# Performance work log

Hardware: AMD Instinct MI355X
Metric: run time of the kernel (lower is better)

The kernel has to match this reference:

```python
import jax, jax.numpy as jnp
import numpy as np

BATCH, DIN, HID = 32768, 64, 1024


def setup_inputs() -> dict:
    key = jax.random.key(0)
    ks = jax.random.split(key, 8)
    s_in = 1.0 / np.sqrt(DIN)
    s_h = 1.0 / np.sqrt(HID)
    return {
        "z": jax.random.normal(ks[0], (BATCH, DIN), dtype=jnp.float32),
        # Hamiltonian net: DIN -> HID -> HID -> 1
        "W1": jax.random.normal(ks[1], (DIN, HID), dtype=jnp.float32) * s_in,
        "b1": jnp.zeros((HID,), jnp.float32),
        "W2": jax.random.normal(ks[2], (HID, HID), dtype=jnp.float32) * s_h,
        "b2": jnp.zeros((HID,), jnp.float32),
        "W3": jax.random.normal(ks[3], (HID, 1), dtype=jnp.float32) * s_h,
        "b3": jnp.zeros((1,), jnp.float32),
        # Forcing net: DIN -> HID -> DIN
        "Wf1": jax.random.normal(ks[4], (DIN, HID), dtype=jnp.float32) * s_in,
        "bf1": jnp.zeros((HID,), jnp.float32),
        "Wf2": jax.random.normal(ks[5], (HID, DIN), dtype=jnp.float32) * s_h,
        "bf2": jnp.zeros((DIN,), jnp.float32),
    }


def reference(z, W1, b1, W2, b2, W3, b3, Wf1, bf1, Wf2, bf2):
    def H_sum(zz):
        h1 = jnp.tanh(zz @ W1 + b1)          # [B, HID]
        h2 = jnp.tanh(h1 @ W2 + b2)          # [B, HID]
        return jnp.sum(h2 @ W3 + b3)         # scalar (sum of H over batch)

    gradH = jax.grad(H_sum)(z)               # [B, DIN]
    dim = z.shape[1] // 2
    # symplectic combine: dq/dt = dH/dp, dp/dt = -dH/dq
    hnn_term = jnp.concatenate([gradH[:, dim:], -gradH[:, :dim]], axis=-1)
    forcing_term = jnp.tanh(z @ Wf1 + bf1) @ Wf2 + bf2  # [B, DIN]
    return hnn_term + forcing_term
```

## Files before the change

### kernel.cpp

```cpp
#include <hip/hip_runtime.h>


typedef __attribute__((ext_vector_type(8))) short s16x8;
typedef __attribute__((ext_vector_type(4))) float f32x4;
typedef unsigned short u16;

#define DEVFN static __device__ __forceinline__

constexpr int DIN = 64;
constexpr int HID = 1024;

DEVFN u16 f2bf(float f) {
  unsigned u = __builtin_bit_cast(unsigned, f);
  u += 0x7fffu + ((u >> 16) & 1u);
  return (u16)(u >> 16);
}
DEVFN float bf2f(u16 h) {
  unsigned u = ((unsigned)h) << 16;
  return __builtin_bit_cast(float, u);
}
DEVFN float fast_tanh(float x) {
  float e = __builtin_amdgcn_exp2f(x * 2.8853900817779268f);
  return 1.0f - 2.0f * __builtin_amdgcn_rcpf(e + 1.0f);
}
DEVFN f32x4 mfma16(s16x8 a, s16x8 b, f32x4 c) {
  return __builtin_amdgcn_mfma_f32_16x16x32_bf16(a, b, c, 0, 0, 0);
}

#define GLOAD16(g, l) __builtin_amdgcn_global_load_lds( \
    (const __attribute__((address_space(1))) unsigned int*)(const void*)(g), \
    (__attribute__((address_space(3))) unsigned int*)(void*)(l), 16, 0, 0)

__global__ __launch_bounds__(256) void k0_w2(const float* __restrict__ W2,
                                             u16* __restrict__ W2tp, u16* __restrict__ W2c) {
  __shared__ u16 tl[64 * 65];
  const int bi = blockIdx.x >> 4, bj = blockIdx.x & 15;
  const int tid = threadIdx.x;
#pragma unroll
  for (int i = 0; i < 16; ++i) {
    int idx = i * 256 + tid;
    int r = idx >> 6, c = idx & 63;
    float v = W2[(size_t)(bi * 64 + r) * 1024 + bj * 64 + c];
    u16 b = f2bf(v);
    W2c[(size_t)(bi * 64 + r) * 1024 + bj * 64 + c] = b;
    tl[r * 65 + c] = b;
  }
  __syncthreads();
#pragma unroll
  for (int i = 0; i < 16; ++i) {
    int idx = i * 256 + tid;
    int r = idx >> 6, c = idx & 63;
    W2tp[(size_t)(bj * 64 + r) * 1024 + bi * 64 + c] = tl[c * 65 + r];
  }
}

__global__ __launch_bounds__(256) void k0_small(
    const float* W1, const float* Wf1, const float* Wf2,
    u16* W1p, u16* Wf1p, u16* W1s, u16* Wf2p) {
  int id = blockIdx.x * 256 + threadIdx.x;
  int n = id >> 6, k = id & 63;
  W1p[id]  = f2bf(W1[k * HID + n]);
  Wf1p[id] = f2bf(Wf1[k * HID + n]);
  int nn = id >> 10, kk2 = id & 1023;
  float s = (nn < 32) ? 1.f : -1.f;
  W1s[id]  = f2bf(s * W1[((nn + 32) & 63) * HID + kk2]);
  Wf2p[id] = f2bf(Wf2[kk2 * DIN + nn]);
}

__global__ __launch_bounds__(256) void k1_h1(const float* z, const u16* Wp,
                                             const float* b, u16* o) {
  __shared__ __align__(16) u16 zl[64 * 72];
  const int tid = threadIdx.x;
  const int lane = tid & 63, w = tid >> 6;
  const int nb = blockIdx.x & 7, mb = blockIdx.x >> 3;
  const size_t m0 = (size_t)mb * 64;
  const int n0 = nb * 128;
#pragma unroll
  for (int c = 0; c < 4; ++c) {
    int i4 = c * 256 + tid;
    int row = i4 >> 4, col4 = (i4 & 15) * 4;
    f32x4 v = *reinterpret_cast<const f32x4*>(z + (m0 + row) * DIN + col4);
    u16* d = zl + row * 72 + col4;
    d[0] = f2bf(v[0]); d[1] = f2bf(v[1]); d[2] = f2bf(v[2]); d[3] = f2bf(v[3]);
  }
  __syncthreads();
  f32x4 acc[8] = {};
#pragma unroll
  for (int kk = 0; kk < 2; ++kk) {
    const int karr = kk * 32 + ((lane >> 4) << 3);
    s16x8 a = *reinterpret_cast<const s16x8*>(zl + (16 * w + (lane & 15)) * 72 + karr);
#pragma unroll
    for (int fn = 0; fn < 8; ++fn) {
      int n = n0 + fn * 16 + (lane & 15);
      s16x8 bb = *reinterpret_cast<const s16x8*>(Wp + (size_t)n * 64 + karr);
      acc[fn] = mfma16(a, bb, acc[fn]);
    }
  }
#pragma unroll
  for (int fn = 0; fn < 8; ++fn) {
    int n = n0 + fn * 16 + (lane & 15);
    float bias = b[n];
#pragma unroll
    for (int j = 0; j < 4; ++j) {
      size_t m = m0 + 16 * w + ((lane >> 4) << 2) + j;
      o[m * HID + n] = f2bf(fast_tanh(acc[fn][j] + bias));
    }
  }
}

template <int MODE>
__global__ __launch_bounds__(512, 2) void k23_gemm(
    const u16* __restrict__ A, const u16* __restrict__ Bp,
    const float* __restrict__ b2, const float* __restrict__ W3,
    const u16* __restrict__ h1in, u16* __restrict__ outb) {
  extern __shared__ u16 lds[];
  const int tid = threadIdx.x;
  const int lane = tid & 63, w = tid >> 6;
  const int wr = w >> 2, wc = w & 3;
  const int xcd = blockIdx.x & 7, local = blockIdx.x >> 3;
  const size_t m0 = (size_t)(xcd * 16 + (local >> 2)) * 256;
  const int n0 = (local & 3) * 256;

  const u16* gpa[4]; const u16* gpb[4]; int lo[4];
#pragma unroll
  for (int c = 0; c < 4; ++c) {
    int idx = c * 512 + tid, row = idx >> 3, cg = idx & 7;
    int sc = (cg ^ (row & 7)) << 3;
    gpa[c] = A + (m0 + row) * 1024 + sc;
    gpb[c] = Bp + (size_t)(n0 + row) * 1024 + sc;
    lo[c] = idx * 8;
  }
#define STAGE_A(B_, T_) { _Pragma("unroll") for (int c = 0; c < 4; ++c) \
    GLOAD16(gpa[c] + (T_) * 64, lds + (B_) * 32768 + lo[c]); }
#define STAGE_B(B_, T_) { _Pragma("unroll") for (int c = 0; c < 4; ++c) \
    GLOAD16(gpb[c] + (T_) * 64, lds + (B_) * 32768 + 16384 + lo[c]); }

  const int swz = (lane & 7) << 3;
  int aoff[8], boff[4];
#pragma unroll
  for (int i = 0; i < 8; ++i)
    aoff[i] = (wr * 128 + i * 16 + (lane & 15)) * 64 + ((lane >> 4) << 3);
#pragma unroll
  for (int j = 0; j < 4; ++j)
    boff[j] = (wc * 64 + j * 16 + (lane & 15)) * 64 + ((lane >> 4) << 3);

  f32x4 acc[8][4] = {};

#define PHASE(B_, KK_) { \
    s16x8 af[8], bf[4]; \
    _Pragma("unroll") for (int i = 0; i < 8; ++i) \
      af[i] = *reinterpret_cast<const s16x8*>(lds + (B_) * 32768 + ((aoff[i] + (KK_) * 32) ^ swz)); \
    _Pragma("unroll") for (int j = 0; j < 4; ++j) \
      bf[j] = *reinterpret_cast<const s16x8*>(lds + (B_) * 32768 + 16384 + ((boff[j] + (KK_) * 32) ^ swz)); \
    __builtin_amdgcn_s_setprio(1); \
    _Pragma("unroll") for (int i = 0; i < 8; ++i) { \
      _Pragma("unroll") for (int j = 0; j < 4; ++j) \
        acc[i][j] = mfma16(af[i], bf[j], acc[i][j]); } \
    __builtin_amdgcn_s_setprio(0); }

  STAGE_A(0, 0); STAGE_B(0, 0);
  for (int t = 0; t < 15; ++t) {
    const int cur = t & 1, nxt = cur ^ 1;
    STAGE_A(nxt, t + 1);
    asm volatile("s_waitcnt vmcnt(4)" ::: "memory");
    __builtin_amdgcn_s_barrier();
    asm volatile("" ::: "memory");
    PHASE(cur, 0);
    STAGE_B(nxt, t + 1);
    PHASE(cur, 1);
    asm volatile("" ::: "memory");
    __builtin_amdgcn_s_barrier();
    asm volatile("" ::: "memory");
  }
  asm volatile("s_waitcnt vmcnt(0)" ::: "memory");
  __builtin_amdgcn_s_barrier();
  asm volatile("" ::: "memory");
  PHASE(1, 0);
  PHASE(1, 1);
  asm volatile("" ::: "memory");
  __builtin_amdgcn_s_barrier();
  asm volatile("" ::: "memory");

  const int wbase = w * 8192;
  float b2v[4], w3v[4];
  if (MODE == 0) {
#pragma unroll
    for (int j = 0; j < 4; ++j) {
      int n = n0 + wc * 64 + j * 16 + (lane & 15);
      b2v[j] = b2[n]; w3v[j] = W3[n];
    }
  }
#pragma unroll
  for (int h = 0; h < 2; ++h) {
    if (h == 1) asm volatile("s_waitcnt lgkmcnt(0)" ::: "memory");
#pragma unroll
    for (int ip = 0; ip < 4; ++ip) {
#pragma unroll
      for (int j = 0; j < 4; ++j) {
#pragma unroll
        for (int r = 0; r < 4; ++r) {
          float v = acc[h * 4 + ip][j][r];
          u16 o;
          if (MODE == 0) {
            float tt = fast_tanh(v + b2v[j]);
            o = f2bf(w3v[j] * (1.f - tt * tt));
          } else {
            o = f2bf(v);
          }
          int lr = ip * 16 + ((lane >> 4) << 2) + r;
          lds[wbase + lr * 64 + j * 16 + (lane & 15)] = o;
        }
      }
    }
#pragma unroll
    for (int r8 = 0; r8 < 8; ++r8) {
      int lr = r8 * 8 + (lane >> 3), c8 = (lane & 7) * 8;
      s16x8 vv = *reinterpret_cast<const s16x8*>(lds + wbase + lr * 64 + c8);
      size_t grow = m0 + wr * 128 + h * 64 + lr;
      int gcol = n0 + wc * 64 + c8;
      if (MODE == 1) {
        s16x8 hh = *reinterpret_cast<const s16x8*>(h1in + grow * 1024 + gcol);
#pragma unroll
        for (int e = 0; e < 8; ++e) {
          float hv = bf2f((u16)hh[e]);
          vv[e] = (short)f2bf(bf2f((u16)vv[e]) * (1.f - hv * hv));
        }
      }
      *reinterpret_cast<s16x8*>(outb + grow * 1024 + gcol) = vv;
    }
  }
#undef STAGE_A
#undef STAGE_B
#undef PHASE
}

__global__ __launch_bounds__(256) void k4_gemm(
    const u16* __restrict__ gp1, const u16* __restrict__ f1,
    const u16* __restrict__ W1s, const u16* __restrict__ Wf2p,
    const float* __restrict__ bf2, float* __restrict__ out) {
  __shared__ __align__(16) u16 Ab[4][4096];
  __shared__ __align__(16) u16 Bb[4][4096];
  const int tid = threadIdx.x;
  const int lane = tid & 63, w = tid >> 6;
  const int lr = lane & 15, g = lane >> 4;
  const size_t m0 = (size_t)blockIdx.x * 64;

  int aoffs[2], boffs[2], lo[2];
#pragma unroll
  for (int c = 0; c < 2; ++c) {
    int idx = c * 256 + tid;
    int row = idx >> 3, cg = idx & 7;
    aoffs[c] = (int)((m0 + row) * 1024) + ((cg ^ (row & 7)) << 3);
    boffs[c] = row * 1024 + ((cg ^ (row & 7)) << 3);
    lo[c] = idx * 8;
  }
#define K4STAGE(B_, T_) { \
    const u16* ab_ = (T_) < 16 ? gp1 : f1; \
    const u16* bb_ = (T_) < 16 ? W1s : Wf2p; \
    const int ko_ = ((T_) & 15) * 64; \
    _Pragma("unroll") for (int c = 0; c < 2; ++c) { \
      GLOAD16(ab_ + aoffs[c] + ko_, Ab[B_] + lo[c]); \
      GLOAD16(bb_ + boffs[c] + ko_, Bb[B_] + lo[c]); } }

  const int arow = w * 16 + lr;
  int afr[2], bfr[2][4];
#pragma unroll
  for (int kkl = 0; kkl < 2; ++kkl) {
    afr[kkl] = arow * 64 + ((kkl * 32 + g * 8) ^ ((arow & 7) << 3));
#pragma unroll
    for (int fn = 0; fn < 4; ++fn) {
      int br = fn * 16 + lr;
      bfr[kkl][fn] = br * 64 + ((kkl * 32 + g * 8) ^ ((br & 7) << 3));
    }
  }

  f32x4 acc[4] = {};
#define K4MM(BUF_) { \
    _Pragma("unroll") for (int kkl = 0; kkl < 2; ++kkl) { \
      s16x8 a = *reinterpret_cast<const s16x8*>(Ab[BUF_] + afr[kkl]); \
      _Pragma("unroll") for (int fn = 0; fn < 4; ++fn) { \
        s16x8 b = *reinterpret_cast<const s16x8*>(Bb[BUF_] + bfr[kkl][fn]); \
        acc[fn] = mfma16(a, b, acc[fn]); } } }
#define TBAR() { asm volatile("" ::: "memory"); __builtin_amdgcn_s_barrier(); asm volatile("" ::: "memory"); }

  K4STAGE(0, 0); K4STAGE(1, 1); K4STAGE(2, 2);
  for (int t = 0; t < 29; ++t) {
    K4STAGE((t + 3) & 3, t + 3);
    asm volatile("s_waitcnt vmcnt(8)" ::: "memory");
    TBAR();
    K4MM(t & 3);
    TBAR();
  }
  K4MM(1);
  TBAR();
  asm volatile("s_waitcnt vmcnt(4)" ::: "memory");
  TBAR();
  K4MM(2);
  TBAR();
  asm volatile("s_waitcnt vmcnt(0)" ::: "memory");
  TBAR();
  K4MM(3);

#pragma unroll
  for (int fn = 0; fn < 4; ++fn) {
    int n = fn * 16 + lr;
    float bias = bf2[n];
#pragma unroll
    for (int j = 0; j < 4; ++j) {
      size_t m = m0 + w * 16 + g * 4 + j;
      out[m * DIN + n] = acc[fn][j] + bias;
    }
  }
#undef K4STAGE
#undef K4MM
#undef TBAR
}

extern "C" void kernel_launch(void* const* d_in, const int* in_sizes, int n_in,
                              void* d_out, int out_size, void* d_ws, size_t ws_size,
                              hipStream_t stream) {
  const float* z   = (const float*)d_in[0];
  const float* W1  = (const float*)d_in[1];
  const float* b1  = (const float*)d_in[2];
  const float* W2  = (const float*)d_in[3];
  const float* b2  = (const float*)d_in[4];
  const float* W3  = (const float*)d_in[5];
  const float* Wf1 = (const float*)d_in[7];
  const float* bf1 = (const float*)d_in[8];
  const float* Wf2 = (const float*)d_in[9];
  const float* bf2 = (const float*)d_in[10];

  char* ws = (char*)d_ws;
  u16* W1p  = (u16*)(ws + 0);
  u16* Wf1p = (u16*)(ws + 131072);
  u16* W2tp = (u16*)(ws + 262144);
  u16* W2c  = (u16*)(ws + 2359296);
  u16* W1s  = (u16*)(ws + 4456448);
  u16* Wf2p = (u16*)(ws + 4587520);
  u16* h1   = (u16*)(ws + 4718592);
  u16* gp2  = (u16*)(ws + 4718592 + 67108864);
  float* out = (float*)d_out;

  k0_w2<<<256, 256, 0, stream>>>(W2, W2tp, W2c);
  k0_small<<<256, 256, 0, stream>>>(W1, Wf1, Wf2, W1p, Wf1p, W1s, Wf2p);
  k1_h1<<<4096, 256, 0, stream>>>(z, W1p, b1, h1);
  k23_gemm<0><<<512, 512, 131072, stream>>>(h1, W2tp, b2, W3, nullptr, gp2);
  k23_gemm<1><<<512, 512, 131072, stream>>>(gp2, W2c, nullptr, nullptr, h1, h1);
  k1_h1<<<4096, 256, 0, stream>>>(z, Wf1p, bf1, gp2);
  k4_gemm<<<512, 256, 0, stream>>>(h1, gp2, W1s, Wf2p, bf2, out);
}
```

Baseline: 254.0 us.

## Halve k23 K-tile with unswizzled LDS and split k4 K-loop across two wave groups

The main 1024x1024 GEMM kernels drop from a 64-wide to a 32-wide K tile per stage, halving LDS per block and removing the XOR swizzle. The A fragments are now loaded in two halves, which lowers register pressure. The final small GEMM kernel moves to 512 threads: two wave groups each handle one of the two concatenated K-halves (gradient path and forcing path) in parallel, and their partial sums are reduced through LDS. The unswizzled 64-byte row stride risks LDS bank conflicts, and the shorter K tiles double the number of barrier iterations.

```diff
diff --git a/kernel.cpp b/kernel.cpp
--- a/kernel.cpp
+++ b/kernel.cpp
@@ -121,53 +121,53 @@
   const size_t m0 = (size_t)(xcd * 16 + (local >> 2)) * 256;
   const int n0 = (local & 3) * 256;
 
-  const u16* gpa[4]; const u16* gpb[4]; int lo[4];
-#pragma unroll
-  for (int c = 0; c < 4; ++c) {
-    int idx = c * 512 + tid, row = idx >> 3, cg = idx & 7;
-    int sc = (cg ^ (row & 7)) << 3;
-    gpa[c] = A + (m0 + row) * 1024 + sc;
-    gpb[c] = Bp + (size_t)(n0 + row) * 1024 + sc;
+  const u16* gpa[2]; const u16* gpb[2]; int lo[2];
+#pragma unroll
+  for (int c = 0; c < 2; ++c) {
+    int idx = c * 512 + tid, row = idx >> 2, cg = idx & 3;
+    gpa[c] = A + (m0 + row) * 1024 + cg * 8;
+    gpb[c] = Bp + (size_t)(n0 + row) * 1024 + cg * 8;
     lo[c] = idx * 8;
   }
-#define STAGE_A(B_, T_) { _Pragma("unroll") for (int c = 0; c < 4; ++c) \
-    GLOAD16(gpa[c] + (T_) * 64, lds + (B_) * 32768 + lo[c]); }
-#define STAGE_B(B_, T_) { _Pragma("unroll") for (int c = 0; c < 4; ++c) \
-    GLOAD16(gpb[c] + (T_) * 64, lds + (B_) * 32768 + 16384 + lo[c]); }
-
-  const int swz = (lane & 7) << 3;
+#define STAGE_A(B_, T_) { _Pragma("unroll") for (int c = 0; c < 2; ++c) \
+    GLOAD16(gpa[c] + (T_) * 32, lds + (B_) * 16384 + lo[c]); }
+#define STAGE_B(B_, T_) { _Pragma("unroll") for (int c = 0; c < 2; ++c) \
+    GLOAD16(gpb[c] + (T_) * 32, lds + (B_) * 16384 + 8192 + lo[c]); }
+
+  const int lr15 = lane & 15, g = lane >> 4;
   int aoff[8], boff[4];
 #pragma unroll
   for (int i = 0; i < 8; ++i)
-    aoff[i] = (wr * 128 + i * 16 + (lane & 15)) * 64 + ((lane >> 4) << 3);
+    aoff[i] = (wr * 128 + i * 16 + lr15) * 32 + g * 8;
 #pragma unroll
   for (int j = 0; j < 4; ++j)
-    boff[j] = (wc * 64 + j * 16 + (lane & 15)) * 64 + ((lane >> 4) << 3);
+    boff[j] = (wc * 64 + j * 16 + lr15) * 32 + g * 8;
 
   f32x4 acc[8][4] = {};
-
-#define PHASE(B_, KK_) { \
-    s16x8 af[8], bf[4]; \
-    _Pragma("unroll") for (int i = 0; i < 8; ++i) \
-      af[i] = *reinterpret_cast<const s16x8*>(lds + (B_) * 32768 + ((aoff[i] + (KK_) * 32) ^ swz)); \
-    _Pragma("unroll") for (int j = 0; j < 4; ++j) \
-      bf[j] = *reinterpret_cast<const s16x8*>(lds + (B_) * 32768 + 16384 + ((boff[j] + (KK_) * 32) ^ swz)); \
-    __builtin_amdgcn_s_setprio(1); \
-    _Pragma("unroll") for (int i = 0; i < 8; ++i) { \
+  s16x8 af[4], bf[4];
+
+#define LDB(B_) { _Pragma("unroll") for (int j = 0; j < 4; ++j) \
+    bf[j] = *reinterpret_cast<const s16x8*>(lds + (B_) * 16384 + 8192 + boff[j]); }
+#define LDA(B_, H_) { _Pragma("unroll") for (int i = 0; i < 4; ++i) \
+    af[i] = *reinterpret_cast<const s16x8*>(lds + (B_) * 16384 + aoff[(H_) * 4 + i]); }
+#define MMH(H_) { __builtin_amdgcn_s_setprio(1); \
+    _Pragma("unroll") for (int i = 0; i < 4; ++i) { \
       _Pragma("unroll") for (int j = 0; j < 4; ++j) \
-        acc[i][j] = mfma16(af[i], bf[j], acc[i][j]); } \
+        acc[(H_) * 4 + i][j] = mfma16(af[i], bf[j], acc[(H_) * 4 + i][j]); } \
     __builtin_amdgcn_s_setprio(0); }
 
   STAGE_A(0, 0); STAGE_B(0, 0);
-  for (int t = 0; t < 15; ++t) {
+  for (int t = 0; t < 31; ++t) {
     const int cur = t & 1, nxt = cur ^ 1;
     STAGE_A(nxt, t + 1);
-    asm volatile("s_waitcnt vmcnt(4)" ::: "memory");
+    asm volatile("s_waitcnt vmcnt(2)" ::: "memory");
     __builtin_amdgcn_s_barrier();
     asm volatile("" ::: "memory");
-    PHASE(cur, 0);
+    LDB(cur); LDA(cur, 0);
+    MMH(0);
     STAGE_B(nxt, t + 1);
-    PHASE(cur, 1);
+    LDA(cur, 1);
+    MMH(1);
     asm volatile("" ::: "memory");
     __builtin_amdgcn_s_barrier();
     asm volatile("" ::: "memory");
@@ -175,13 +175,15 @@
   asm volatile("s_waitcnt vmcnt(0)" ::: "memory");
   __builtin_amdgcn_s_barrier();
   asm volatile("" ::: "memory");
-  PHASE(1, 0);
-  PHASE(1, 1);
+  LDB(1); LDA(1, 0);
+  MMH(0);
+  LDA(1, 1);
+  MMH(1);
   asm volatile("" ::: "memory");
   __builtin_amdgcn_s_barrier();
   asm volatile("" ::: "memory");
 
-  const int wbase = w * 8192;
+  const int wbase = w * 4096;
   float b2v[4], w3v[4];
   if (MODE == 0) {
 #pragma unroll
@@ -231,36 +233,39 @@
   }
 #undef STAGE_A
 #undef STAGE_B
-#undef PHASE
-}
-
-__global__ __launch_bounds__(256) void k4_gemm(
+#undef LDB
+#undef LDA
+#undef MMH
+}
+
+__global__ __launch_bounds__(512) void k4_gemm(
     const u16* __restrict__ gp1, const u16* __restrict__ f1,
     const u16* __restrict__ W1s, const u16* __restrict__ Wf2p,
     const float* __restrict__ bf2, float* __restrict__ out) {
-  __shared__ __align__(16) u16 Ab[4][4096];
-  __shared__ __align__(16) u16 Bb[4][4096];
+  __shared__ __align__(16) u16 Ab[2][2][4096];
+  __shared__ __align__(16) u16 Bb[2][2][4096];
   const int tid = threadIdx.x;
-  const int lane = tid & 63, w = tid >> 6;
+  const int w8 = tid >> 6, lane = tid & 63;
+  const int grp = w8 >> 2, w = w8 & 3;
+  const int gt = tid & 255;
   const int lr = lane & 15, g = lane >> 4;
   const size_t m0 = (size_t)blockIdx.x * 64;
+  const u16* asrc = grp ? f1 : gp1;
+  const u16* bsrc = grp ? Wf2p : W1s;
 
   int aoffs[2], boffs[2], lo[2];
 #pragma unroll
   for (int c = 0; c < 2; ++c) {
-    int idx = c * 256 + tid;
+    int idx = c * 256 + gt;
     int row = idx >> 3, cg = idx & 7;
     aoffs[c] = (int)((m0 + row) * 1024) + ((cg ^ (row & 7)) << 3);
     boffs[c] = row * 1024 + ((cg ^ (row & 7)) << 3);
     lo[c] = idx * 8;
   }
-#define K4STAGE(B_, T_) { \
-    const u16* ab_ = (T_) < 16 ? gp1 : f1; \
-    const u16* bb_ = (T_) < 16 ? W1s : Wf2p; \
-    const int ko_ = ((T_) & 15) * 64; \
+#define K4STAGE(B_, T_) { const int ko_ = (T_) * 64; \
     _Pragma("unroll") for (int c = 0; c < 2; ++c) { \
-      GLOAD16(ab_ + aoffs[c] + ko_, Ab[B_] + lo[c]); \
-      GLOAD16(bb_ + boffs[c] + ko_, Bb[B_] + lo[c]); } }
+      GLOAD16(asrc + aoffs[c] + ko_, Ab[grp][B_] + lo[c]); \
+      GLOAD16(bsrc + boffs[c] + ko_, Bb[grp][B_] + lo[c]); } }
 
   const int arow = w * 16 + lr;
   int afr[2], bfr[2][4];
@@ -277,38 +282,45 @@
   f32x4 acc[4] = {};
 #define K4MM(BUF_) { \
     _Pragma("unroll") for (int kkl = 0; kkl < 2; ++kkl) { \
-      s16x8 a = *reinterpret_cast<const s16x8*>(Ab[BUF_] + afr[kkl]); \
+      s16x8 a = *reinterpret_cast<const s16x8*>(Ab[grp][BUF_] + afr[kkl]); \
       _Pragma("unroll") for (int fn = 0; fn < 4; ++fn) { \
-        s16x8 b = *reinterpret_cast<const s16x8*>(Bb[BUF_] + bfr[kkl][fn]); \
+        s16x8 b = *reinterpret_cast<const s16x8*>(Bb[grp][BUF_] + bfr[kkl][fn]); \
         acc[fn] = mfma16(a, b, acc[fn]); } } }
 #define TBAR() { asm volatile("" ::: "memory"); __builtin_amdgcn_s_barrier(); asm volatile("" ::: "memory"); }
 
-  K4STAGE(0, 0); K4STAGE(1, 1); K4STAGE(2, 2);
-  for (int t = 0; t < 29; ++t) {
-    K4STAGE((t + 3) & 3, t + 3);
-    asm volatile("s_waitcnt vmcnt(8)" ::: "memory");
+  K4STAGE(0, 0);
+  for (int t = 0; t < 15; ++t) {
+    K4STAGE((t + 1) & 1, t + 1);
+    asm volatile("s_waitcnt vmcnt(4)" ::: "memory");
     TBAR();
-    K4MM(t & 3);
+    K4MM(t & 1);
     TBAR();
   }
-  K4MM(1);
-  TBAR();
-  asm volatile("s_waitcnt vmcnt(4)" ::: "memory");
-  TBAR();
-  K4MM(2);
-  TBAR();
   asm volatile("s_waitcnt vmcnt(0)" ::: "memory");
   TBAR();
-  K4MM(3);
-
-#pragma unroll
-  for (int fn = 0; fn < 4; ++fn) {
-    int n = fn * 16 + lr;
-    float bias = bf2[n];
-#pragma unroll
-    for (int j = 0; j < 4; ++j) {
-      size_t m = m0 + w * 16 + g * 4 + j;
-      out[m * DIN + n] = acc[fn][j] + bias;
+  K4MM(1);
+
+  __syncthreads();
+  float* red = (float*)&Ab[0][0][0];
+  if (grp == 1) {
+#pragma unroll
+    for (int fn = 0; fn < 4; ++fn)
+#pragma unroll
+      for (int j = 0; j < 4; ++j)
+        red[(fn * 4 + j) * 256 + gt] = acc[fn][j];
+  }
+  __syncthreads();
+  if (grp == 0) {
+#pragma unroll
+    for (int fn = 0; fn < 4; ++fn) {
+      int n = fn * 16 + lr;
+      float bias = bf2[n];
+#pragma unroll
+      for (int j = 0; j < 4; ++j) {
+        float v = acc[fn][j] + red[(fn * 4 + j) * 256 + gt] + bias;
+        size_t m = m0 + w * 16 + g * 4 + j;
+        out[m * DIN + n] = v;
+      }
     }
   }
 #undef K4STAGE
@@ -344,8 +356,8 @@
   k0_w2<<<256, 256, 0, stream>>>(W2, W2tp, W2c);
   k0_small<<<256, 256, 0, stream>>>(W1, Wf1, Wf2, W1p, Wf1p, W1s, Wf2p);
   k1_h1<<<4096, 256, 0, stream>>>(z, W1p, b1, h1);
-  k23_gemm<0><<<512, 512, 131072, stream>>>(h1, W2tp, b2, W3, nullptr, gp2);
-  k23_gemm<1><<<512, 512, 131072, stream>>>(gp2, W2c, nullptr, nullptr, h1, h1);
+  k23_gemm<0><<<512, 512, 65536, stream>>>(h1, W2tp, b2, W3, nullptr, gp2);
+  k23_gemm<1><<<512, 512, 65536, stream>>>(gp2, W2c, nullptr, nullptr, h1, h1);
   k1_h1<<<4096, 256, 0, stream>>>(z, Wf1p, bf1, gp2);
-  k4_gemm<<<512, 256, 0, stream>>>(h1, gp2, W1s, Wf2p, bf2, out);
-}
+  k4_gemm<<<512, 512, 0, stream>>>(h1, gp2, W1s, Wf2p, bf2, out);
+}
```

Result: slower. 266.9 us (+5.1%).

## Split k4 GEMM K-range across two wave groups and merge weight-prep kernels

Applied to the files above, without the earlier changes.

The final GEMM now runs 512 threads per block, with two 256-thread groups each handling one of the two concatenated K halves (the HNN gradient path and the forcing path) in their own double-buffered LDS pipeline. Partial accumulators are reduced through shared memory before the bias is added and the result stored. This halves the serial K loop per wave, targeting latency in a kernel that had only 512 small blocks. In exchange, pipeline depth drops from four stages to two and an LDS reduction is added. Separately, the two weight-conversion kernels are fused into one launch to save a kernel launch.

```diff
diff --git a/kernel.cpp b/kernel.cpp
--- a/kernel.cpp
+++ b/kernel.cpp
@@ -31,8 +31,12 @@
     (const __attribute__((address_space(1))) unsigned int*)(const void*)(g), \
     (__attribute__((address_space(3))) unsigned int*)(void*)(l), 16, 0, 0)
 
-__global__ __launch_bounds__(256) void k0_w2(const float* __restrict__ W2,
-                                             u16* __restrict__ W2tp, u16* __restrict__ W2c) {
+__global__ __launch_bounds__(256) void k0_prep(
+    const float* __restrict__ W2, const float* __restrict__ W1,
+    const float* __restrict__ Wf1, const float* __restrict__ Wf2,
+    u16* __restrict__ W2tp, u16* __restrict__ W2c,
+    u16* __restrict__ W1p, u16* __restrict__ Wf1p,
+    u16* __restrict__ W1s, u16* __restrict__ Wf2p) {
   __shared__ u16 tl[64 * 65];
   const int bi = blockIdx.x >> 4, bj = blockIdx.x & 15;
   const int tid = threadIdx.x;
@@ -52,12 +56,7 @@
     int r = idx >> 6, c = idx & 63;
     W2tp[(size_t)(bj * 64 + r) * 1024 + bi * 64 + c] = tl[c * 65 + r];
   }
-}
-
-__global__ __launch_bounds__(256) void k0_small(
-    const float* W1, const float* Wf1, const float* Wf2,
-    u16* W1p, u16* Wf1p, u16* W1s, u16* Wf2p) {
-  int id = blockIdx.x * 256 + threadIdx.x;
+  int id = blockIdx.x * 256 + tid;
   int n = id >> 6, k = id & 63;
   W1p[id]  = f2bf(W1[k * HID + n]);
   Wf1p[id] = f2bf(Wf1[k * HID + n]);
@@ -234,33 +233,34 @@
 #undef PHASE
 }
 
-__global__ __launch_bounds__(256) void k4_gemm(
+__global__ __launch_bounds__(512) void k4_gemm(
     const u16* __restrict__ gp1, const u16* __restrict__ f1,
     const u16* __restrict__ W1s, const u16* __restrict__ Wf2p,
     const float* __restrict__ bf2, float* __restrict__ out) {
-  __shared__ __align__(16) u16 Ab[4][4096];
-  __shared__ __align__(16) u16 Bb[4][4096];
+  __shared__ __align__(16) u16 Ab[2][2][4096];
+  __shared__ __align__(16) u16 Bb[2][2][4096];
   const int tid = threadIdx.x;
-  const int lane = tid & 63, w = tid >> 6;
+  const int w8 = tid >> 6, lane = tid & 63;
+  const int grp = w8 >> 2, w = w8 & 3;
+  const int gt = tid & 255;
   const int lr = lane & 15, g = lane >> 4;
   const size_t m0 = (size_t)blockIdx.x * 64;
+  const u16* asrc = grp ? f1 : gp1;
+  const u16* bsrc = grp ? Wf2p : W1s;
 
   int aoffs[2], boffs[2], lo[2];
 #pragma unroll
   for (int c = 0; c < 2; ++c) {
-    int idx = c * 256 + tid;
+    int idx = c * 256 + gt;
     int row = idx >> 3, cg = idx & 7;
     aoffs[c] = (int)((m0 + row) * 1024) + ((cg ^ (row & 7)) << 3);
     boffs[c] = row * 1024 + ((cg ^ (row & 7)) << 3);
     lo[c] = idx * 8;
   }
-#define K4STAGE(B_, T_) { \
-    const u16* ab_ = (T_) < 16 ? gp1 : f1; \
-    const u16* bb_ = (T_) < 16 ? W1s : Wf2p; \
-    const int ko_ = ((T_) & 15) * 64; \
+#define K4STAGE(B_, T_) { const int ko_ = (T_) * 64; \
     _Pragma("unroll") for (int c = 0; c < 2; ++c) { \
-      GLOAD16(ab_ + aoffs[c] + ko_, Ab[B_] + lo[c]); \
-      GLOAD16(bb_ + boffs[c] + ko_, Bb[B_] + lo[c]); } }
+      GLOAD16(asrc + aoffs[c] + ko_, Ab[grp][B_] + lo[c]); \
+      GLOAD16(bsrc + boffs[c] + ko_, Bb[grp][B_] + lo[c]); } }
 
   const int arow = w * 16 + lr;
   int afr[2], bfr[2][4];
@@ -277,38 +277,45 @@
   f32x4 acc[4] = {};
 #define K4MM(BUF_) { \
     _Pragma("unroll") for (int kkl = 0; kkl < 2; ++kkl) { \
-      s16x8 a = *reinterpret_cast<const s16x8*>(Ab[BUF_] + afr[kkl]); \
+      s16x8 a = *reinterpret_cast<const s16x8*>(Ab[grp][BUF_] + afr[kkl]); \
       _Pragma("unroll") for (int fn = 0; fn < 4; ++fn) { \
-        s16x8 b = *reinterpret_cast<const s16x8*>(Bb[BUF_] + bfr[kkl][fn]); \
+        s16x8 b = *reinterpret_cast<const s16x8*>(Bb[grp][BUF_] + bfr[kkl][fn]); \
         acc[fn] = mfma16(a, b, acc[fn]); } } }
 #define TBAR() { asm volatile("" ::: "memory"); __builtin_amdgcn_s_barrier(); asm volatile("" ::: "memory"); }
 
-  K4STAGE(0, 0); K4STAGE(1, 1); K4STAGE(2, 2);
-  for (int t = 0; t < 29; ++t) {
-    K4STAGE((t + 3) & 3, t + 3);
-    asm volatile("s_waitcnt vmcnt(8)" ::: "memory");
+  K4STAGE(0, 0);
+  for (int t = 0; t < 15; ++t) {
+    K4STAGE((t + 1) & 1, t + 1);
+    asm volatile("s_waitcnt vmcnt(4)" ::: "memory");
     TBAR();
-    K4MM(t & 3);
+    K4MM(t & 1);
     TBAR();
   }
-  K4MM(1);
-  TBAR();
-  asm volatile("s_waitcnt vmcnt(4)" ::: "memory");
-  TBAR();
-  K4MM(2);
-  TBAR();
   asm volatile("s_waitcnt vmcnt(0)" ::: "memory");
   TBAR();
-  K4MM(3);
-
-#pragma unroll
-  for (int fn = 0; fn < 4; ++fn) {
-    int n = fn * 16 + lr;
-    float bias = bf2[n];
-#pragma unroll
-    for (int j = 0; j < 4; ++j) {
-      size_t m = m0 + w * 16 + g * 4 + j;
-      out[m * DIN + n] = acc[fn][j] + bias;
+  K4MM(1);
+
+  __syncthreads();
+  float* red = (float*)&Ab[0][0][0];
+  if (grp == 1) {
+#pragma unroll
+    for (int fn = 0; fn < 4; ++fn)
+#pragma unroll
+      for (int j = 0; j < 4; ++j)
+        red[(fn * 4 + j) * 256 + gt] = acc[fn][j];
+  }
+  __syncthreads();
+  if (grp == 0) {
+#pragma unroll
+    for (int fn = 0; fn < 4; ++fn) {
+      int n = fn * 16 + lr;
+      float bias = bf2[n];
+#pragma unroll
+      for (int j = 0; j < 4; ++j) {
+        float v = acc[fn][j] + red[(fn * 4 + j) * 256 + gt] + bias;
+        size_t m = m0 + w * 16 + g * 4 + j;
+        out[m * DIN + n] = v;
+      }
     }
   }
 #undef K4STAGE
@@ -341,11 +348,10 @@
   u16* gp2  = (u16*)(ws + 4718592 + 67108864);
   float* out = (float*)d_out;
 
-  k0_w2<<<256, 256, 0, stream>>>(W2, W2tp, W2c);
-  k0_small<<<256, 256, 0, stream>>>(W1, Wf1, Wf2, W1p, Wf1p, W1s, Wf2p);
+  k0_prep<<<256, 256, 0, stream>>>(W2, W1, Wf1, Wf2, W2tp, W2c, W1p, Wf1p, W1s, Wf2p);
   k1_h1<<<4096, 256, 0, stream>>>(z, W1p, b1, h1);
   k23_gemm<0><<<512, 512, 131072, stream>>>(h1, W2tp, b2, W3, nullptr, gp2);
   k23_gemm<1><<<512, 512, 131072, stream>>>(gp2, W2c, nullptr, nullptr, h1, h1);
   k1_h1<<<4096, 256, 0, stream>>>(z, Wf1p, bf1, gp2);
-  k4_gemm<<<512, 256, 0, stream>>>(h1, gp2, W1s, Wf2p, bf2, out);
-}
+  k4_gemm<<<512, 512, 0, stream>>>(h1, gp2, W1s, Wf2p, bf2, out);
+}
```

Result: no change. 251.5 us (-1.0%).
